# Kernel tuning notes

Measured on AMD Instinct MI355X. Metric: run time of the kernel, lower is better.

## Reference

```python
import jax, jax.numpy as jnp
import numpy as np

Q, N, D = 4096, 50000, 64

def setup_inputs() -> dict:
    key = jax.random.key(0)
    k1, k2, k3, k4 = jax.random.split(key, 4)
    features = jax.random.normal(k1, (Q, D), dtype=jnp.float32)
    # bw_transform is a (lower-triangular cholesky) bandwidth transform; a small
    # random matrix is fine for a numerical reference. Scale down so exp(-d2/2)
    # does not underflow everywhere.
    bw_transform = jax.random.normal(k2, (D, D), dtype=jnp.float32) * 0.05
    dataset = jax.random.normal(k3, (N, D), dtype=jnp.float32)
    norm = jax.random.uniform(k4, (1,), dtype=jnp.float32)
    return {"features": features, "bw_transform": bw_transform, "dataset": dataset, "norm": norm}

def reference(features, bw_transform, dataset, norm):
    # features: [Q, D], bw_transform: [D, D], dataset: [N, D] (already transformed), norm: [1]
    f = features @ bw_transform  # [Q, D]
    # pairwise squared distances via expansion: ||f||^2 + ||x||^2 - 2 f.x
    f2 = jnp.sum(f * f, axis=1)            # [Q]
    x2 = jnp.sum(dataset * dataset, axis=1)  # [N]
    d2 = f2[:, None] + x2[None, :] - 2.0 * (f @ dataset.T)  # [Q, N]
    kern = jnp.exp(-0.5 * d2) * norm[0]    # [Q, N]
    estimate = jnp.mean(kern, axis=1)       # [Q]
    return estimate
```

## Files before the change

kernel.cpp:

```cpp
#include <hip/hip_runtime.h>


#define QCNT 4096
#define NCNT 50000
#define DDIM 64

#define SPLITS 64
#define NPB 832
#define NROWS (SPLITS * NPB)
#define NUNITS 26
#define QTILES (QCNT / 256)
#define SPLIT_HALVES (NPB * DDIM)

#define FSPLITS 32
#define FNPB 1563
#define FNITERS 25
#define BN 64

typedef _Float16 half8_t __attribute__((ext_vector_type(8)));
typedef float float4_t __attribute__((ext_vector_type(4)));

#define K2F 1.44269504088896340f
#define KC2 -0.72134752044448169f

#define PREP_F_BLOCKS (QCNT / 4)
#define PREP_X_BLOCKS (NROWS * 8 / 256)

__global__ void prep_fused(const float* __restrict__ features,
                           const float* __restrict__ bw,
                           const float* __restrict__ dataset,
                           _Float16* __restrict__ fh,
                           float* __restrict__ cf2,
                           _Float16* __restrict__ xhp,
                           float* __restrict__ ecxg) {
    if (blockIdx.x < PREP_F_BLOCKS) {
        const int lane = threadIdx.x & 63;
        const int q = blockIdx.x * 4 + (threadIdx.x >> 6);
        const float* frow = features + q * DDIM;
        float acc = 0.f;
#pragma unroll
        for (int k = 0; k < DDIM; ++k)
            acc = fmaf(frow[k], bw[k * DDIM + lane], acc);
        fh[(size_t)q * DDIM + lane] = (_Float16)(K2F * acc);
        float s = acc * acc;
#pragma unroll
        for (int m = 1; m < 64; m <<= 1) s += __shfl_xor(s, m, 64);
        if (lane == 0) cf2[q] = KC2 * s;
    } else {
        const int t = (blockIdx.x - PREP_F_BLOCKS) * 256 + threadIdx.x;
        const int row = t >> 3;
        const int c = t & 7;
        if (row >= NROWS) return;
        float4_t v0 = {0.f, 0.f, 0.f, 0.f}, v1 = {0.f, 0.f, 0.f, 0.f};
        if (row < NCNT) {
            const float4_t* src = (const float4_t*)(dataset + (size_t)row * DDIM + c * 8);
            v0 = src[0]; v1 = src[1];
        }
        float s = v0[0]*v0[0] + v0[1]*v0[1] + v0[2]*v0[2] + v0[3]*v0[3]
                + v1[0]*v1[0] + v1[1]*v1[1] + v1[2]*v1[2] + v1[3]*v1[3];
        s += __shfl_xor(s, 1, 64);
        s += __shfl_xor(s, 2, 64);
        s += __shfl_xor(s, 4, 64);
        if (c == 0) ecxg[row] = (row < NCNT) ? __builtin_amdgcn_exp2f(KC2 * s) : 0.f;
        half8_t h;
        h[0] = (_Float16)v0[0]; h[1] = (_Float16)v0[1];
        h[2] = (_Float16)v0[2]; h[3] = (_Float16)v0[3];
        h[4] = (_Float16)v1[0]; h[5] = (_Float16)v1[1];
        h[6] = (_Float16)v1[2]; h[7] = (_Float16)v1[3];
        const int split = row / NPB;
        const int nr = row - split * NPB;
        const int it = nr >> 6;
        const int brow = nr & 63;
        const int nt = brow >> 4;
        const int l15 = brow & 15;
        const int f = c >> 2;
        const int lh = c & 3;
        const int lane = lh * 16 + l15;
        const size_t base = ((((size_t)split * 13 + it) * 4 + nt) * 2 + f) * 512;
        *(half8_t*)(xhp + base + lane * 8) = h;
    }
}

__global__ __launch_bounds__(256, 4)
void kde_main_fast(const _Float16* __restrict__ fh,
                   const float* __restrict__ ecxg,
                   const _Float16* __restrict__ xhp,
                   float* __restrict__ partial) {
    __shared__ float lecx[NPB];

    const int tid = threadIdx.x;
    const int lane = tid & 63;
    const int w = tid >> 6;
    const int l15 = lane & 15;
    const int lh = lane >> 4;

    const int bid = blockIdx.x;
    const int xcd = bid & 7;
    const int j = bid >> 3;
    const int split = xcd * 8 + (j & 7);
    const int qtile = j >> 3;

    const int qbase = qtile * 256 + w * 64;

    half8_t a[4][2];
#pragma unroll
    for (int qt = 0; qt < 4; ++qt)
#pragma unroll
        for (int kt = 0; kt < 2; ++kt)
            a[qt][kt] = *(const half8_t*)(fh + (size_t)(qbase + qt * 16 + l15) * DDIM
                                             + kt * 32 + lh * 8);

    {
        const float* es = ecxg + (size_t)split * NPB;
        for (int i = tid; i < NPB; i += 256) lecx[i] = es[i];
    }
    __syncthreads();

    {
        const int skew = w + ((bid >> 3) & 3);
#pragma unroll 1
        for (int i = 0; i < skew; ++i) __builtin_amdgcn_s_sleep(2);
    }

    const _Float16* bs = xhp + (size_t)split * SPLIT_HALVES + (size_t)lane * 8;

    float sum[4][4];
#pragma unroll
    for (int qt = 0; qt < 4; ++qt)
#pragma unroll
        for (int r = 0; r < 4; ++r) sum[qt][r] = 0.f;

    const float4_t zc = {0.f, 0.f, 0.f, 0.f};

#define LOADU(P, u_)                                                          \
    {                                                                         \
        const _Float16* p_ = bs + (size_t)(u_) * 2048;                        \
        P[0][0] = *(const half8_t*)(p_);                                      \
        P[0][1] = *(const half8_t*)(p_ + 512);                                \
        P[1][0] = *(const half8_t*)(p_ + 1024);                               \
        P[1][1] = *(const half8_t*)(p_ + 1536);                               \
    }

#define COMPU(P, u_)                                                          \
    {                                                                         \
        _Pragma("unroll")                                                     \
        for (int s_ = 0; s_ < 2; ++s_) {                                      \
            const float e_ = lecx[(u_) * 32 + s_ * 16 + l15];                 \
            float4_t t0, t1, t2, t3;                                          \
            __builtin_amdgcn_s_setprio(1);                                    \
            t0 = __builtin_amdgcn_mfma_f32_16x16x32_f16(a[0][0], P[s_][0], zc, 0, 0, 0); \
            t1 = __builtin_amdgcn_mfma_f32_16x16x32_f16(a[1][0], P[s_][0], zc, 0, 0, 0); \
            t2 = __builtin_amdgcn_mfma_f32_16x16x32_f16(a[2][0], P[s_][0], zc, 0, 0, 0); \
            t3 = __builtin_amdgcn_mfma_f32_16x16x32_f16(a[3][0], P[s_][0], zc, 0, 0, 0); \
            t0 = __builtin_amdgcn_mfma_f32_16x16x32_f16(a[0][1], P[s_][1], t0, 0, 0, 0); \
            t1 = __builtin_amdgcn_mfma_f32_16x16x32_f16(a[1][1], P[s_][1], t1, 0, 0, 0); \
            t2 = __builtin_amdgcn_mfma_f32_16x16x32_f16(a[2][1], P[s_][1], t2, 0, 0, 0); \
            t3 = __builtin_amdgcn_mfma_f32_16x16x32_f16(a[3][1], P[s_][1], t3, 0, 0, 0); \
            __builtin_amdgcn_s_setprio(0);                                    \
            _Pragma("unroll")                                                 \
            for (int r = 0; r < 4; ++r) {                                     \
                sum[0][r] = fmaf(__builtin_amdgcn_exp2f(t0[r]), e_, sum[0][r]); \
                sum[1][r] = fmaf(__builtin_amdgcn_exp2f(t1[r]), e_, sum[1][r]); \
                sum[2][r] = fmaf(__builtin_amdgcn_exp2f(t2[r]), e_, sum[2][r]); \
                sum[3][r] = fmaf(__builtin_amdgcn_exp2f(t3[r]), e_, sum[3][r]); \
            }                                                                 \
        }                                                                     \
    }

    half8_t bA[2][2], bB[2][2];

    LOADU(bA, 0);
#pragma unroll 1
    for (int u = 0; u < NUNITS; u += 2) {
        LOADU(bB, u + 1);
        COMPU(bA, u);
        if (u + 2 < NUNITS) LOADU(bA, u + 2);
        COMPU(bB, u + 1);
    }

#pragma unroll
    for (int qt = 0; qt < 4; ++qt)
#pragma unroll
        for (int r = 0; r < 4; ++r) {
            float s = sum[qt][r];
            s += __shfl_xor(s, 1, 64);
            s += __shfl_xor(s, 2, 64);
            s += __shfl_xor(s, 4, 64);
            s += __shfl_xor(s, 8, 64);
            sum[qt][r] = s;
        }
    if (l15 == 0) {
        float* dst = partial + (size_t)split * QCNT + qbase;
#pragma unroll
        for (int qt = 0; qt < 4; ++qt)
#pragma unroll
            for (int r = 0; r < 4; ++r)
                dst[qt * 16 + lh * 4 + r] = sum[qt][r];
    }
#undef LOADU
#undef COMPU
}

__global__ void prep_f_kernel(const float* __restrict__ features,
                              const float* __restrict__ bw,
                              _Float16* __restrict__ fh,
                              float* __restrict__ cf2) {
    const int lane = threadIdx.x & 63;
    const int q = blockIdx.x * (blockDim.x >> 6) + (threadIdx.x >> 6);
    if (q >= QCNT) return;
    const float* frow = features + q * DDIM;
    float acc = 0.f;
#pragma unroll
    for (int k = 0; k < DDIM; ++k)
        acc = fmaf(frow[k], bw[k * DDIM + lane], acc);
    fh[(size_t)q * DDIM + lane] = (_Float16)(K2F * acc);
    float s = acc * acc;
#pragma unroll
    for (int m = 1; m < 64; m <<= 1) s += __shfl_xor(s, m, 64);
    if (lane == 0) cf2[q] = KC2 * s;
}

__global__ void prep_x2_kernel(const float* __restrict__ dataset,
                               float* __restrict__ cx2) {
    const int n = blockIdx.x * blockDim.x + threadIdx.x;
    if (n >= NCNT) return;
    const float4* row = (const float4*)(dataset + (size_t)n * DDIM);
    float s = 0.f;
#pragma unroll
    for (int jq = 0; jq < DDIM / 4; ++jq) {
        float4 v = row[jq];
        s += v.x * v.x + v.y * v.y + v.z * v.z + v.w * v.w;
    }
    cx2[n] = KC2 * s;
}

__global__ __launch_bounds__(256, 2)
void kde_main_fb(const _Float16* __restrict__ fh,
                 const float* __restrict__ cx2,
                 const float* __restrict__ dataset,
                 float* __restrict__ partial) {
    __shared__ __align__(16) _Float16 xt[BN * DDIM];
    const int tid = threadIdx.x;
    const int lane = tid & 63;
    const int w = tid >> 6;
    const int l15 = lane & 15;
    const int lh = lane >> 4;
    const int qbase = blockIdx.x * 256 + w * 64;
    const int nstart = blockIdx.y * FNPB;
    const int nlimit = min(nstart + FNPB, NCNT);

    half8_t a[4][2];
#pragma unroll
    for (int qt = 0; qt < 4; ++qt)
#pragma unroll
        for (int kt = 0; kt < 2; ++kt)
            a[qt][kt] = *(const half8_t*)(fh + (size_t)(qbase + qt * 16 + l15) * DDIM
                                             + kt * 32 + lh * 8);
    float sum[4][4];
#pragma unroll
    for (int qt = 0; qt < 4; ++qt)
#pragma unroll
        for (int r = 0; r < 4; ++r) sum[qt][r] = 0.f;

    const int sn = tid >> 2;
    const int sk = tid & 3;
    const int c0 = (sk * 2) ^ (sn & 7);
    const int c1 = (sk * 2 + 1) ^ (sn & 7);

    for (int it = 0; it < FNITERS; ++it) {
        const int nb = nstart + it * BN;
        __syncthreads();
        {
            const int ng = nb + sn;
            float4_t v0 = {0.f,0.f,0.f,0.f}, v1 = {0.f,0.f,0.f,0.f};
            float4_t v2 = {0.f,0.f,0.f,0.f}, v3 = {0.f,0.f,0.f,0.f};
            if (ng < nlimit) {
                const float4_t* src = (const float4_t*)(dataset + (size_t)ng * DDIM + sk * 16);
                v0 = src[0]; v1 = src[1]; v2 = src[2]; v3 = src[3];
            }
            half8_t h0, h1;
            h0[0]=(_Float16)v0[0]; h0[1]=(_Float16)v0[1]; h0[2]=(_Float16)v0[2]; h0[3]=(_Float16)v0[3];
            h0[4]=(_Float16)v1[0]; h0[5]=(_Float16)v1[1]; h0[6]=(_Float16)v1[2]; h0[7]=(_Float16)v1[3];
            h1[0]=(_Float16)v2[0]; h1[1]=(_Float16)v2[1]; h1[2]=(_Float16)v2[2]; h1[3]=(_Float16)v2[3];
            h1[4]=(_Float16)v3[0]; h1[5]=(_Float16)v3[1]; h1[6]=(_Float16)v3[2]; h1[7]=(_Float16)v3[3];
            *(half8_t*)(xt + sn * DDIM + c0 * 8) = h0;
            *(half8_t*)(xt + sn * DDIM + c1 * 8) = h1;
        }
        __syncthreads();
#pragma unroll
        for (int nt = 0; nt < 4; ++nt) {
            const int ng = nb + nt * 16 + l15;
            const float c2 = (ng < nlimit) ? cx2[ng] : -1.0e30f;
            const int brow = nt * 16 + l15;
            const half8_t b0 = *(const half8_t*)(xt + brow * DDIM + ((lh ^ (brow & 7)) * 8));
            const half8_t b1 = *(const half8_t*)(xt + brow * DDIM + (((4 + lh) ^ (brow & 7)) * 8));
#pragma unroll
            for (int qt = 0; qt < 4; ++qt) {
                float4_t c = {c2, c2, c2, c2};
                float4_t acc = __builtin_amdgcn_mfma_f32_16x16x32_f16(a[qt][0], b0, c, 0, 0, 0);
                acc = __builtin_amdgcn_mfma_f32_16x16x32_f16(a[qt][1], b1, acc, 0, 0, 0);
#pragma unroll
                for (int r = 0; r < 4; ++r)
                    sum[qt][r] += __builtin_amdgcn_exp2f(acc[r]);
            }
        }
    }
#pragma unroll
    for (int qt = 0; qt < 4; ++qt)
#pragma unroll
        for (int r = 0; r < 4; ++r) {
            float s = sum[qt][r];
            s += __shfl_xor(s, 1, 64);
            s += __shfl_xor(s, 2, 64);
            s += __shfl_xor(s, 4, 64);
            s += __shfl_xor(s, 8, 64);
            sum[qt][r] = s;
        }
    if (l15 == 0) {
        float* dst = partial + (size_t)blockIdx.y * QCNT + qbase;
#pragma unroll
        for (int qt = 0; qt < 4; ++qt)
#pragma unroll
            for (int r = 0; r < 4; ++r)
                dst[qt * 16 + lh * 4 + r] = sum[qt][r];
    }
}

__global__ void reduce_kernel(const float* __restrict__ partial,
                              const float* __restrict__ cf2,
                              const float* __restrict__ norm,
                              float* __restrict__ out, int splits) {
    const int t = blockIdx.x * blockDim.x + threadIdx.x;
    const int q = t >> 2;
    const int sub = t & 3;
    if (q >= QCNT) return;
    const int per = splits >> 2;
    float s = 0.f;
    for (int sp = sub * per; sp < (sub + 1) * per; ++sp)
        s += partial[(size_t)sp * QCNT + q];
    s += __shfl_xor(s, 1, 64);
    s += __shfl_xor(s, 2, 64);
    if (sub == 0)
        out[q] = s * __builtin_amdgcn_exp2f(cf2[q]) * norm[0] * (1.0f / (float)NCNT);
}

extern "C" void kernel_launch(void* const* d_in, const int* in_sizes, int n_in,
                              void* d_out, int out_size, void* d_ws, size_t ws_size,
                              hipStream_t stream) {
    const float* features = (const float*)d_in[0];
    const float* bw       = (const float*)d_in[1];
    const float* dataset  = (const float*)d_in[2];
    const float* norm     = (const float*)d_in[3];
    float* out = (float*)d_out;
    float* ws = (float*)d_ws;

    const size_t NEED = (size_t)(1703936 + 131072 + 4096 + 53248 + 262144) * 4;

    if (ws_size >= NEED) {
        _Float16* xhp = (_Float16*)ws;
        _Float16* fh  = (_Float16*)(ws + 1703936);
        float* cf2     = ws + 1703936 + 131072;
        float* ecxg    = cf2 + 4096;
        float* partial = ecxg + 53248;

        prep_fused<<<PREP_F_BLOCKS + PREP_X_BLOCKS, 256, 0, stream>>>(
            features, bw, dataset, fh, cf2, xhp, ecxg);
        kde_main_fast<<<QTILES * SPLITS, 256, 0, stream>>>(fh, ecxg, xhp, partial);
        reduce_kernel<<<(QCNT * 4) / 256, 256, 0, stream>>>(partial, cf2, norm, out, SPLITS);
    } else {
        _Float16* fh = (_Float16*)ws;
        float* cf2     = ws + 131072;
        float* cx2     = ws + 131072 + 4096;
        float* partial = ws + 131072 + 4096 + 50176;

        prep_f_kernel<<<QCNT / 4, 256, 0, stream>>>(features, bw, fh, cf2);
        prep_x2_kernel<<<(NCNT + 255) / 256, 256, 0, stream>>>(dataset, cx2);
        dim3 grid(QCNT / 256, FSPLITS);
        kde_main_fb<<<grid, 256, 0, stream>>>(fh, cx2, dataset, partial);
        reduce_kernel<<<(QCNT * 4) / 256, 256, 0, stream>>>(partial, cf2, norm, out, FSPLITS);
    }
}
```

Measured before the change: 55.65 us.

## Software-pipeline MFMA and exp stages across 16-row halves in KDE main loop

Restructures the main loop into 16-row half units so the MFMA for one half is issued while exp/accumulate of the previous half runs, with loads two halves ahead. This is meant to overlap matrix-core work with transcendental VALU work instead of serialising them within each unit. The dataset packing layout is simplified to match the per-half indexing (same physical layout). Launch bounds are replaced with explicit waves-per-EU attributes pinning occupancy at 4, which may change register allocation.

```diff
diff --git a/kernel.cpp b/kernel.cpp
--- a/kernel.cpp
+++ b/kernel.cpp
@@ -8,7 +8,7 @@
 #define SPLITS 64
 #define NPB 832
 #define NROWS (SPLITS * NPB)
-#define NUNITS 26
+#define NHALVES 52
 #define QTILES (QCNT / 256)
 #define SPLIT_HALVES (NPB * DDIM)
 
@@ -69,19 +69,18 @@
         h[6] = (_Float16)v1[2]; h[7] = (_Float16)v1[3];
         const int split = row / NPB;
         const int nr = row - split * NPB;
-        const int it = nr >> 6;
-        const int brow = nr & 63;
-        const int nt = brow >> 4;
-        const int l15 = brow & 15;
+        const int hh = nr >> 4;
+        const int l15 = nr & 15;
         const int f = c >> 2;
         const int lh = c & 3;
         const int lane = lh * 16 + l15;
-        const size_t base = ((((size_t)split * 13 + it) * 4 + nt) * 2 + f) * 512;
+        const size_t base = (((size_t)split * NHALVES + hh) * 2 + f) * 512;
         *(half8_t*)(xhp + base + lane * 8) = h;
     }
 }
 
-__global__ __launch_bounds__(256, 4)
+__global__ __attribute__((amdgpu_flat_work_group_size(256, 256),
+                          amdgpu_waves_per_eu(4, 4)))
 void kde_main_fast(const _Float16* __restrict__ fh,
                    const float* __restrict__ ecxg,
                    const _Float16* __restrict__ xhp,
@@ -132,51 +131,64 @@
 
     const float4_t zc = {0.f, 0.f, 0.f, 0.f};
 
-#define LOADU(P, u_)                                                          \
+#define LOADH(L, h_)                                                          \
     {                                                                         \
-        const _Float16* p_ = bs + (size_t)(u_) * 2048;                        \
-        P[0][0] = *(const half8_t*)(p_);                                      \
-        P[0][1] = *(const half8_t*)(p_ + 512);                                \
-        P[1][0] = *(const half8_t*)(p_ + 1024);                               \
-        P[1][1] = *(const half8_t*)(p_ + 1536);                               \
-    }
-
-#define COMPU(P, u_)                                                          \
+        const _Float16* p_ = bs + (size_t)(h_) * 1024;                        \
+        L[0] = *(const half8_t*)(p_);                                         \
+        L[1] = *(const half8_t*)(p_ + 512);                                   \
+    }
+
+#define MFMAH(T, L)                                                           \
     {                                                                         \
+        __builtin_amdgcn_s_setprio(1);                                        \
+        T[0] = __builtin_amdgcn_mfma_f32_16x16x32_f16(a[0][0], L[0], zc, 0, 0, 0); \
+        T[1] = __builtin_amdgcn_mfma_f32_16x16x32_f16(a[1][0], L[0], zc, 0, 0, 0); \
+        T[2] = __builtin_amdgcn_mfma_f32_16x16x32_f16(a[2][0], L[0], zc, 0, 0, 0); \
+        T[3] = __builtin_amdgcn_mfma_f32_16x16x32_f16(a[3][0], L[0], zc, 0, 0, 0); \
+        T[0] = __builtin_amdgcn_mfma_f32_16x16x32_f16(a[0][1], L[1], T[0], 0, 0, 0); \
+        T[1] = __builtin_amdgcn_mfma_f32_16x16x32_f16(a[1][1], L[1], T[1], 0, 0, 0); \
+        T[2] = __builtin_amdgcn_mfma_f32_16x16x32_f16(a[2][1], L[1], T[2], 0, 0, 0); \
+        T[3] = __builtin_amdgcn_mfma_f32_16x16x32_f16(a[3][1], L[1], T[3], 0, 0, 0); \
+        __builtin_amdgcn_s_setprio(0);                                        \
+    }
+
+#define EXPH(T, h_)                                                           \
+    {                                                                         \
+        const float e_ = lecx[(h_) * 16 + l15];                               \
         _Pragma("unroll")                                                     \
-        for (int s_ = 0; s_ < 2; ++s_) {                                      \
-            const float e_ = lecx[(u_) * 32 + s_ * 16 + l15];                 \
-            float4_t t0, t1, t2, t3;                                          \
-            __builtin_amdgcn_s_setprio(1);                                    \
-            t0 = __builtin_amdgcn_mfma_f32_16x16x32_f16(a[0][0], P[s_][0], zc, 0, 0, 0); \
-            t1 = __builtin_amdgcn_mfma_f32_16x16x32_f16(a[1][0], P[s_][0], zc, 0, 0, 0); \
-            t2 = __builtin_amdgcn_mfma_f32_16x16x32_f16(a[2][0], P[s_][0], zc, 0, 0, 0); \
-            t3 = __builtin_amdgcn_mfma_f32_16x16x32_f16(a[3][0], P[s_][0], zc, 0, 0, 0); \
-            t0 = __builtin_amdgcn_mfma_f32_16x16x32_f16(a[0][1], P[s_][1], t0, 0, 0, 0); \
-            t1 = __builtin_amdgcn_mfma_f32_16x16x32_f16(a[1][1], P[s_][1], t1, 0, 0, 0); \
-            t2 = __builtin_amdgcn_mfma_f32_16x16x32_f16(a[2][1], P[s_][1], t2, 0, 0, 0); \
-            t3 = __builtin_amdgcn_mfma_f32_16x16x32_f16(a[3][1], P[s_][1], t3, 0, 0, 0); \
-            __builtin_amdgcn_s_setprio(0);                                    \
-            _Pragma("unroll")                                                 \
-            for (int r = 0; r < 4; ++r) {                                     \
-                sum[0][r] = fmaf(__builtin_amdgcn_exp2f(t0[r]), e_, sum[0][r]); \
-                sum[1][r] = fmaf(__builtin_amdgcn_exp2f(t1[r]), e_, sum[1][r]); \
-                sum[2][r] = fmaf(__builtin_amdgcn_exp2f(t2[r]), e_, sum[2][r]); \
-                sum[3][r] = fmaf(__builtin_amdgcn_exp2f(t3[r]), e_, sum[3][r]); \
-            }                                                                 \
+        for (int r = 0; r < 4; ++r) {                                         \
+            sum[0][r] = fmaf(__builtin_amdgcn_exp2f(T[0][r]), e_, sum[0][r]); \
+            sum[1][r] = fmaf(__builtin_amdgcn_exp2f(T[1][r]), e_, sum[1][r]); \
+            sum[2][r] = fmaf(__builtin_amdgcn_exp2f(T[2][r]), e_, sum[2][r]); \
+            sum[3][r] = fmaf(__builtin_amdgcn_exp2f(T[3][r]), e_, sum[3][r]); \
         }                                                                     \
     }
 
-    half8_t bA[2][2], bB[2][2];
-
-    LOADU(bA, 0);
+    half8_t lA[2], lB[2];
+    float4_t tA[4], tB[4];
+
+    LOADH(lA, 0);
+    LOADH(lB, 1);
+    MFMAH(tA, lA);
+    LOADH(lA, 2);
+
 #pragma unroll 1
-    for (int u = 0; u < NUNITS; u += 2) {
-        LOADU(bB, u + 1);
-        COMPU(bA, u);
-        if (u + 2 < NUNITS) LOADU(bA, u + 2);
-        COMPU(bB, u + 1);
-    }
+    for (int h = 0; h < NHALVES - 4; h += 2) {
+        MFMAH(tB, lB);
+        EXPH(tA, h);
+        LOADH(lB, h + 3);
+        MFMAH(tA, lA);
+        EXPH(tB, h + 1);
+        LOADH(lA, h + 4);
+    }
+    MFMAH(tB, lB);
+    EXPH(tA, 48);
+    LOADH(lB, 51);
+    MFMAH(tA, lA);
+    EXPH(tB, 49);
+    MFMAH(tB, lB);
+    EXPH(tA, 50);
+    EXPH(tB, 51);
 
 #pragma unroll
     for (int qt = 0; qt < 4; ++qt)
@@ -197,8 +209,9 @@
             for (int r = 0; r < 4; ++r)
                 dst[qt * 16 + lh * 4 + r] = sum[qt][r];
     }
-#undef LOADU
-#undef COMPU
+#undef LOADH
+#undef MFMAH
+#undef EXPH
 }
 
 __global__ void prep_f_kernel(const float* __restrict__ features,
```

Measured after the change: 54.97 us, median of 3. About the same (-1.2%).
